# Performance work log

Hardware: AMD Instinct MI355X
Metric: run time of the kernel (lower is better)

## Reference

```python
import jax, jax.numpy as jnp
import numpy as np

EPS = 1e-7  # K.epsilon()
ROUTINGS = 3

def squash(x, axis=-1):
    s2 = jnp.sum(jnp.square(x), axis=axis, keepdims=True)
    scale = s2 / (1.0 + s2) / jnp.sqrt(s2 + EPS)
    return scale * x

def setup_inputs() -> dict:
    key = jax.random.key(0)
    k1, k2 = jax.random.split(key)
    B, N, Di = 64, 1152, 16   # batch, n_input_capsules, dim_input_capsule
    C, Dc = 32, 32            # n_capsules, dim_capsule
    inputs = jax.random.normal(k1, (B, N, Di), dtype=jnp.float32)
    # glorot-style scale for stability
    W = jax.random.normal(k2, (C, N, Dc, Di), dtype=jnp.float32) * (1.0 / np.sqrt(Di))
    return {"inputs": inputs, "W": W}

def reference(inputs, W):
    # inputs: [B, N, Di]; W: [C, N, Dc, Di]
    # inputs_hat[b,c,n,j] = sum_i inputs[b,n,i] * W[c,n,j,i]
    u_hat = jnp.einsum('bni,cnji->bcnj', inputs, W)  # [B, C, N, Dc]
    B, C, N, Dc = u_hat.shape
    b = jnp.zeros((B, C, N), dtype=u_hat.dtype)
    outputs = None
    for i in range(ROUTINGS):
        c = jax.nn.softmax(b, axis=1)                 # softmax over output capsules
        s = jnp.einsum('bcn,bcnj->bcj', c, u_hat)     # weighted sum over input caps
        outputs = squash(s)                           # [B, C, Dc]
        if i < ROUTINGS - 1:
            b = b + jnp.einsum('bcj,bcnj->bcn', outputs, u_hat)
    return outputs
```

## Files before the change

kernel.cpp:

```cpp
#include <hip/hip_runtime.h>
#include <math.h>

using bh8    = __attribute__((ext_vector_type(8))) short;
using f32x16 = __attribute__((ext_vector_type(16))) float;
typedef unsigned int u32;

#define NN   1152
#define CCAP 32
#define DI   16
#define DCAP 32
#define TNR  9
#define NTILES 128
#define CAPS_EPS 1e-7f

#define LDS_W    0
#define LDS_X    65536
#define LDS_DU   74752
#define LDS_CF   78976
#define LDS_TOT  83200

#define WS_WB    0ul
#define WS_XB    37748736ul
#define WS_PART  40108032ul
#define WS_PART2 73662464ul
#define WS_OPK   77856768ul
#define WS_BLOG  77987840ul

__device__ __forceinline__ short f2bf(float f) {
    u32 u = __float_as_uint(f);
    u += 0x7fffu + ((u >> 16) & 1u);
    return (short)(u >> 16);
}

__device__ __forceinline__ void gld_lds16(const void* g, void* s) {
    __builtin_amdgcn_global_load_lds(
        (const __attribute__((address_space(1))) u32*)g,
        (__attribute__((address_space(3))) u32*)s, 16, 0, 0);
}

__global__ __launch_bounds__(256)
void conv_w(const float* __restrict__ W, short* __restrict__ Wb)
{
    const int m = blockIdx.x * 256 + threadIdx.x;
    const int l = m & 63, c = (m >> 6) & 31, n = m >> 11;
    const int j = l & 31, hi = l >> 5;
    const float* src = W + (((size_t)c * NN + n) * DCAP + j) * DI + hi * 8;
    const float4 a = ((const float4*)src)[0];
    const float4 b = ((const float4*)src)[1];
    bh8 r;
    r[0] = f2bf(a.x); r[1] = f2bf(a.y); r[2] = f2bf(a.z); r[3] = f2bf(a.w);
    r[4] = f2bf(b.x); r[5] = f2bf(b.y); r[6] = f2bf(b.z); r[7] = f2bf(b.w);
    *(bh8*)(Wb + (size_t)m * 8) = r;
}

__global__ __launch_bounds__(256)
void conv_x(const float* __restrict__ X, short* __restrict__ xb)
{
    const int m = blockIdx.x * 256 + threadIdx.x;
    const int l = m & 63;
    const int h = m / (NN * 64);
    const int n = (m >> 6) % NN;
    const int b = h * 32 + (l & 31), hi = l >> 5;
    const float* src = X + ((size_t)b * NN + n) * DI + hi * 8;
    const float4 a = ((const float4*)src)[0];
    const float4 c4 = ((const float4*)src)[1];
    bh8 r;
    r[0] = f2bf(a.x);  r[1] = f2bf(a.y);  r[2] = f2bf(a.z);  r[3] = f2bf(a.w);
    r[4] = f2bf(c4.x); r[5] = f2bf(c4.y); r[6] = f2bf(c4.z); r[7] = f2bf(c4.w);
    *(bh8*)(xb + (size_t)m * 8) = r;
}

template<int T>
__global__ __launch_bounds__(512, 2)
void route_k(const short* __restrict__ Wb, const short* __restrict__ xb,
             const u32* __restrict__ opk, float* __restrict__ blog,
             float* __restrict__ part)
{
    extern __shared__ char smem[];
    const int tid = threadIdx.x;
    const int w = tid >> 6, l = tid & 63, bl31 = l & 31;
    const int nt = blockIdx.x, h = blockIdx.y;
    const int n0 = nt * TNR;
    const int bk = h * NTILES + nt;

    char* Wl  = smem + LDS_W;
    char* Xl  = smem + LDS_X;
    float* DU = (float*)(smem + LDS_DU);
    float* CF = (float*)(smem + LDS_CF);

    {
        const char* xs = (const char*)(xb + ((size_t)h * NN + n0) * 512);
        gld_lds16(xs + tid * 16, Xl + tid * 16);
        if (tid < 64) gld_lds16(xs + (512 + tid) * 16, Xl + (512 + tid) * 16);
    }
    {
        const char* wsrc = (const char*)(Wb + (size_t)n0 * 16384);
#pragma unroll
        for (int k = 0; k < 4; ++k)
            gld_lds16(wsrc + (k * 512 + tid) * 16, Wl + (k * 512 + tid) * 16);
    }

    uint4 opr[4][2];
    if (T > 0) {
#pragma unroll
        for (int cc = 0; cc < 4; ++cc) {
            const int c = w * 4 + cc;
            const char* ob = (const char*)opk;
            opr[cc][0] = *(const uint4*)(ob + ((((size_t)h * CCAP + c) * 2 + 0) * 64 + l) * 16);
            opr[cc][1] = *(const uint4*)(ob + ((((size_t)h * CCAP + c) * 2 + 1) * 64 + l) * 16);
        }
    }
    __syncthreads();

    f32x16 sacc[4];
#pragma unroll
    for (int cc = 0; cc < 4; ++cc)
#pragma unroll
        for (int r = 0; r < 16; ++r) sacc[cc][r] = 0.f;

    for (int n = 0; n < TNR; ++n) {
        const int buf = n & 1;
        const int na = n0 + n;

        if (n + 1 < TNR) {
            const char* wsrc = (const char*)(Wb + (size_t)(na + 1) * 16384);
            char* wdst = Wl + (buf ^ 1) * 32768;
#pragma unroll
            for (int k = 0; k < 4; ++k)
                gld_lds16(wsrc + (k * 512 + tid) * 16, wdst + (k * 512 + tid) * 16);
        }

        const bh8 xf = *(const bh8*)(Xl + n * 1024 + l * 16);
        bh8 wf[4];
#pragma unroll
        for (int cc = 0; cc < 4; ++cc) {
            const int c = w * 4 + cc;
            wf[cc] = *(const bh8*)(Wl + buf * 32768 + (c * 64 + l) * 16);
        }

        if (T == 0) {
#pragma unroll
            for (int cc = 0; cc < 4; ++cc)
                sacc[cc] = __builtin_amdgcn_mfma_f32_32x32x16_bf16(wf[cc], xf, sacc[cc], 0, 0, 0);
        } else {
            f32x16 zz;
#pragma unroll
            for (int r = 0; r < 16; ++r) zz[r] = 0.f;
            f32x16 u[4];
#pragma unroll
            for (int cc = 0; cc < 4; ++cc)
                u[cc] = __builtin_amdgcn_mfma_f32_32x32x16_bf16(wf[cc], xf, zz, 0, 0, 0);

            float du[4];
#pragma unroll
            for (int cc = 0; cc < 4; ++cc) {
                const u32 o[8] = {opr[cc][0].x, opr[cc][0].y, opr[cc][0].z, opr[cc][0].w,
                                  opr[cc][1].x, opr[cc][1].y, opr[cc][1].z, opr[cc][1].w};
                float d = 0.f;
#pragma unroll
                for (int p = 0; p < 8; ++p) {
                    const float e0 = __uint_as_float(o[p] << 16);
                    const float e1 = __uint_as_float(o[p] & 0xffff0000u);
                    d = fmaf(e0, u[cc][2 * p + 0], d);
                    d = fmaf(e1, u[cc][2 * p + 1], d);
                }
                d += __shfl_xor(d, 32);
                const int c = w * 4 + cc;
                if (T == 2) d += blog[(((size_t)na * CCAP + c) * 2 + h) * 32 + bl31];
                du[cc] = d;
            }
#pragma unroll
            for (int cc = 0; cc < 4; ++cc) {
                const int c = w * 4 + cc;
                if (l < 32) {
                    DU[c * 33 + l] = du[cc];
                    if (T == 1) blog[(((size_t)na * CCAP + c) * 2 + h) * 32 + l] = du[cc];
                }
            }
            __syncthreads();

            {
                const int b = tid >> 4, g = tid & 15;
                const float v0 = DU[g * 33 + b], v1 = DU[(g + 16) * 33 + b];
                float m = fmaxf(v0, v1);
#pragma unroll
                for (int d2 = 1; d2 < 16; d2 <<= 1) m = fmaxf(m, __shfl_xor(m, d2));
                const float e0 = __expf(v0 - m), e1 = __expf(v1 - m);
                float es = e0 + e1;
#pragma unroll
                for (int d2 = 1; d2 < 16; d2 <<= 1) es += __shfl_xor(es, d2);
                const float inv = 1.0f / es;
                CF[g * 33 + b] = e0 * inv;
                CF[(g + 16) * 33 + b] = e1 * inv;
            }
            __syncthreads();

#pragma unroll
            for (int cc = 0; cc < 4; ++cc) {
                const int c = w * 4 + cc;
                const float cf = CF[c * 33 + bl31];
#pragma unroll
                for (int r = 0; r < 16; ++r)
                    sacc[cc][r] = fmaf(cf, u[cc][r], sacc[cc][r]);
            }
        }
        if (T == 0) __syncthreads();
    }

#pragma unroll
    for (int cc = 0; cc < 4; ++cc) {
        const int c = w * 4 + cc;
        float* dst = part + (((size_t)bk * CCAP + c) * 64 + l) * 16;
#pragma unroll
        for (int k = 0; k < 4; ++k) {
            float4 v;
            v.x = sacc[cc][4 * k + 0]; v.y = sacc[cc][4 * k + 1];
            v.z = sacc[cc][4 * k + 2]; v.w = sacc[cc][4 * k + 3];
            ((float4*)dst)[k] = v;
        }
    }
}

__global__ __launch_bounds__(1024)
void reduce1_k(const float* __restrict__ part, float* __restrict__ part2)
{
    const int t = threadIdx.x;
    const int ch = blockIdx.x, c = blockIdx.y, h = blockIdx.z;
    float a = 0.f;
#pragma unroll
    for (int s = 0; s < 8; ++s) {
        const int nt = ch * 8 + s;
        a += part[((size_t)(h * NTILES + nt) * CCAP + c) * 1024 + t];
    }
    part2[(((size_t)h * CCAP + c) * 16 + ch) * 1024 + t] = a;
}

template<int FIN>
__global__ __launch_bounds__(1024)
void reduce2_k(const float* __restrict__ part2, u32* __restrict__ opk,
               float* __restrict__ outp, float sc0)
{
    const int t = threadIdx.x;
    const int c = blockIdx.x, h = blockIdx.y;
    const int l = t >> 4, r = t & 15;
    float s = 0.f;
#pragma unroll
    for (int ch = 0; ch < 16; ++ch)
        s += part2[(((size_t)h * CCAP + c) * 16 + ch) * 1024 + t];
    s *= sc0;

    float q = s * s;
    q += __shfl_xor(q, 1); q += __shfl_xor(q, 2);
    q += __shfl_xor(q, 4); q += __shfl_xor(q, 8);
    __shared__ float ssq[64], scl[32];
    if (r == 0) ssq[l] = q;
    __syncthreads();
    if (t < 32) {
        const float v = ssq[t] + ssq[t + 32];
        scl[t] = v / ((1.0f + v) * sqrtf(v + CAPS_EPS));
    }
    __syncthreads();
    const float o = s * scl[l & 31];

    if (FIN) {
        const int b = h * 32 + (l & 31);
        const int j = (r & 3) + 8 * (r >> 2) + 4 * (l >> 5);
        outp[((size_t)b * CCAP + c) * DCAP + j] = o;
    } else {
        const float o1 = __shfl_xor(o, 1);
        if (!(r & 1)) {
            const u32 pk = (u32)(unsigned short)f2bf(o) |
                           ((u32)(unsigned short)f2bf(o1) << 16);
            opk[((((size_t)h * CCAP + c) * 2 + (r >> 3)) * 64 + l) * 4 + ((r >> 1) & 3)] = pk;
        }
    }
}

extern "C" void kernel_launch(void* const* d_in, const int* in_sizes, int n_in,
                              void* d_out, int out_size, void* d_ws, size_t ws_size,
                              hipStream_t stream)
{
    const float* inp = (const float*)d_in[0];
    const float* Wt  = (const float*)d_in[1];
    float* out = (float*)d_out;

    char* ws = (char*)d_ws;
    short* Wb    = (short*)(ws + WS_WB);
    short* xb    = (short*)(ws + WS_XB);
    float* part  = (float*)(ws + WS_PART);
    float* part2 = (float*)(ws + WS_PART2);
    u32*   opk   = (u32*)  (ws + WS_OPK);
    float* blog  = (float*)(ws + WS_BLOG);

    hipFuncSetAttribute((const void*)route_k<0>, hipFuncAttributeMaxDynamicSharedMemorySize, LDS_TOT);
    hipFuncSetAttribute((const void*)route_k<1>, hipFuncAttributeMaxDynamicSharedMemorySize, LDS_TOT);
    hipFuncSetAttribute((const void*)route_k<2>, hipFuncAttributeMaxDynamicSharedMemorySize, LDS_TOT);

    conv_w<<<9216, 256, 0, stream>>>(Wt, Wb);
    conv_x<<<576, 256, 0, stream>>>(inp, xb);

    const dim3 gr(NTILES, 2), br(512);
    const dim3 g1(16, 32, 2);
    const dim3 g2(32, 2);

    route_k<0><<<gr, br, LDS_TOT, stream>>>(Wb, xb, opk, blog, part);
    reduce1_k<<<g1, 1024, 0, stream>>>(part, part2);
    reduce2_k<0><<<g2, 1024, 0, stream>>>(part2, opk, out, 1.0f / 32.0f);

    route_k<1><<<gr, br, LDS_TOT, stream>>>(Wb, xb, opk, blog, part);
    reduce1_k<<<g1, 1024, 0, stream>>>(part, part2);
    reduce2_k<0><<<g2, 1024, 0, stream>>>(part2, opk, out, 1.0f);

    route_k<2><<<gr, br, LDS_TOT, stream>>>(Wb, xb, opk, blog, part);
    reduce1_k<<<g1, 1024, 0, stream>>>(part, part2);
    reduce2_k<1><<<g2, 1024, 0, stream>>>(part2, opk, out, 1.0f);
}
```

Measured before the change: 217.3 us.

## Load W fragments directly to registers and double threads per routing block

The routing kernel stops staging W tiles through double-buffered LDS and instead loads each wave's W fragments straight from global memory into registers, prefetching the next input capsule's fragments. Blocks grow from 512 to 1024 threads, with each wave handling two output capsules instead of four. LDS shrinks to the x tile plus the softmax scratch, which lowers register pressure per wave and raises occupancy. In exchange, W loads no longer use async LDS copies, so global latency must be hidden by the register prefetch and the extra waves. The block-wide barriers now span twice as many waves.

```diff
diff --git a/kernel.cpp b/kernel.cpp
--- a/kernel.cpp
+++ b/kernel.cpp
@@ -12,12 +12,6 @@
 #define TNR  9
 #define NTILES 128
 #define CAPS_EPS 1e-7f
-
-#define LDS_W    0
-#define LDS_X    65536
-#define LDS_DU   74752
-#define LDS_CF   78976
-#define LDS_TOT  83200
 
 #define WS_WB    0ul
 #define WS_XB    37748736ul
@@ -71,115 +65,98 @@
 }
 
 template<int T>
-__global__ __launch_bounds__(512, 2)
+__global__ __launch_bounds__(1024, 4)
 void route_k(const short* __restrict__ Wb, const short* __restrict__ xb,
              const u32* __restrict__ opk, float* __restrict__ blog,
              float* __restrict__ part)
 {
-    extern __shared__ char smem[];
+    __shared__ __align__(16) char Xl[TNR * 1024];
+    __shared__ float DU[CCAP * 33];
+    __shared__ float CF[CCAP * 33];
+
     const int tid = threadIdx.x;
     const int w = tid >> 6, l = tid & 63, bl31 = l & 31;
     const int nt = blockIdx.x, h = blockIdx.y;
     const int n0 = nt * TNR;
     const int bk = h * NTILES + nt;
-
-    char* Wl  = smem + LDS_W;
-    char* Xl  = smem + LDS_X;
-    float* DU = (float*)(smem + LDS_DU);
-    float* CF = (float*)(smem + LDS_CF);
-
-    {
+    const int c0 = w * 2, c1 = c0 + 1;
+
+    if (tid < TNR * 64) {
         const char* xs = (const char*)(xb + ((size_t)h * NN + n0) * 512);
         gld_lds16(xs + tid * 16, Xl + tid * 16);
-        if (tid < 64) gld_lds16(xs + (512 + tid) * 16, Xl + (512 + tid) * 16);
-    }
+    }
+
+    uint4 opr[2][2];
+    if (T > 0) {
+        const char* ob = (const char*)opk;
+        opr[0][0] = *(const uint4*)(ob + ((((size_t)h * CCAP + c0) * 2 + 0) * 64 + l) * 16);
+        opr[0][1] = *(const uint4*)(ob + ((((size_t)h * CCAP + c0) * 2 + 1) * 64 + l) * 16);
+        opr[1][0] = *(const uint4*)(ob + ((((size_t)h * CCAP + c1) * 2 + 0) * 64 + l) * 16);
+        opr[1][1] = *(const uint4*)(ob + ((((size_t)h * CCAP + c1) * 2 + 1) * 64 + l) * 16);
+    }
+
+    bh8 wA0, wA1, wB0, wB1;
     {
-        const char* wsrc = (const char*)(Wb + (size_t)n0 * 16384);
-#pragma unroll
-        for (int k = 0; k < 4; ++k)
-            gld_lds16(wsrc + (k * 512 + tid) * 16, Wl + (k * 512 + tid) * 16);
-    }
-
-    uint4 opr[4][2];
-    if (T > 0) {
-#pragma unroll
-        for (int cc = 0; cc < 4; ++cc) {
-            const int c = w * 4 + cc;
-            const char* ob = (const char*)opk;
-            opr[cc][0] = *(const uint4*)(ob + ((((size_t)h * CCAP + c) * 2 + 0) * 64 + l) * 16);
-            opr[cc][1] = *(const uint4*)(ob + ((((size_t)h * CCAP + c) * 2 + 1) * 64 + l) * 16);
-        }
-    }
+        const short* p = Wb + (size_t)n0 * 16384;
+        wA0 = *(const bh8*)(p + (c0 * 64 + l) * 8);
+        wA1 = *(const bh8*)(p + (c1 * 64 + l) * 8);
+    }
+
+    f32x16 s0, s1;
+#pragma unroll
+    for (int r = 0; r < 16; ++r) { s0[r] = 0.f; s1[r] = 0.f; }
+
     __syncthreads();
 
-    f32x16 sacc[4];
-#pragma unroll
-    for (int cc = 0; cc < 4; ++cc)
-#pragma unroll
-        for (int r = 0; r < 16; ++r) sacc[cc][r] = 0.f;
-
+#pragma unroll
     for (int n = 0; n < TNR; ++n) {
-        const int buf = n & 1;
         const int na = n0 + n;
 
         if (n + 1 < TNR) {
-            const char* wsrc = (const char*)(Wb + (size_t)(na + 1) * 16384);
-            char* wdst = Wl + (buf ^ 1) * 32768;
-#pragma unroll
-            for (int k = 0; k < 4; ++k)
-                gld_lds16(wsrc + (k * 512 + tid) * 16, wdst + (k * 512 + tid) * 16);
+            const short* p = Wb + (size_t)(na + 1) * 16384;
+            wB0 = *(const bh8*)(p + (c0 * 64 + l) * 8);
+            wB1 = *(const bh8*)(p + (c1 * 64 + l) * 8);
         }
 
         const bh8 xf = *(const bh8*)(Xl + n * 1024 + l * 16);
-        bh8 wf[4];
-#pragma unroll
-        for (int cc = 0; cc < 4; ++cc) {
-            const int c = w * 4 + cc;
-            wf[cc] = *(const bh8*)(Wl + buf * 32768 + (c * 64 + l) * 16);
-        }
 
         if (T == 0) {
-#pragma unroll
-            for (int cc = 0; cc < 4; ++cc)
-                sacc[cc] = __builtin_amdgcn_mfma_f32_32x32x16_bf16(wf[cc], xf, sacc[cc], 0, 0, 0);
+            s0 = __builtin_amdgcn_mfma_f32_32x32x16_bf16(wA0, xf, s0, 0, 0, 0);
+            s1 = __builtin_amdgcn_mfma_f32_32x32x16_bf16(wA1, xf, s1, 0, 0, 0);
         } else {
             f32x16 zz;
 #pragma unroll
             for (int r = 0; r < 16; ++r) zz[r] = 0.f;
-            f32x16 u[4];
-#pragma unroll
-            for (int cc = 0; cc < 4; ++cc)
-                u[cc] = __builtin_amdgcn_mfma_f32_32x32x16_bf16(wf[cc], xf, zz, 0, 0, 0);
-
-            float du[4];
-#pragma unroll
-            for (int cc = 0; cc < 4; ++cc) {
-                const u32 o[8] = {opr[cc][0].x, opr[cc][0].y, opr[cc][0].z, opr[cc][0].w,
-                                  opr[cc][1].x, opr[cc][1].y, opr[cc][1].z, opr[cc][1].w};
-                float d = 0.f;
-#pragma unroll
-                for (int p = 0; p < 8; ++p) {
-                    const float e0 = __uint_as_float(o[p] << 16);
-                    const float e1 = __uint_as_float(o[p] & 0xffff0000u);
-                    d = fmaf(e0, u[cc][2 * p + 0], d);
-                    d = fmaf(e1, u[cc][2 * p + 1], d);
+            f32x16 u0 = __builtin_amdgcn_mfma_f32_32x32x16_bf16(wA0, xf, zz, 0, 0, 0);
+            f32x16 u1 = __builtin_amdgcn_mfma_f32_32x32x16_bf16(wA1, xf, zz, 0, 0, 0);
+
+            float d0 = 0.f, d1 = 0.f;
+#pragma unroll
+            for (int p = 0; p < 8; ++p) {
+                const u32 o0 = (p < 4) ? (&opr[0][0].x)[p] : (&opr[0][1].x)[p - 4];
+                const u32 o1 = (p < 4) ? (&opr[1][0].x)[p] : (&opr[1][1].x)[p - 4];
+                d0 = fmaf(__uint_as_float(o0 << 16),        u0[2 * p + 0], d0);
+                d0 = fmaf(__uint_as_float(o0 & 0xffff0000u), u0[2 * p + 1], d0);
+                d1 = fmaf(__uint_as_float(o1 << 16),        u1[2 * p + 0], d1);
+                d1 = fmaf(__uint_as_float(o1 & 0xffff0000u), u1[2 * p + 1], d1);
+            }
+            d0 += __shfl_xor(d0, 32);
+            d1 += __shfl_xor(d1, 32);
+            if (T == 2) {
+                d0 += blog[(((size_t)na * CCAP + c0) * 2 + h) * 32 + bl31];
+                d1 += blog[(((size_t)na * CCAP + c1) * 2 + h) * 32 + bl31];
+            }
+            if (l < 32) {
+                DU[c0 * 33 + l] = d0;
+                DU[c1 * 33 + l] = d1;
+                if (T == 1) {
+                    blog[(((size_t)na * CCAP + c0) * 2 + h) * 32 + l] = d0;
+                    blog[(((size_t)na * CCAP + c1) * 2 + h) * 32 + l] = d1;
                 }
-                d += __shfl_xor(d, 32);
-                const int c = w * 4 + cc;
-                if (T == 2) d += blog[(((size_t)na * CCAP + c) * 2 + h) * 32 + bl31];
-                du[cc] = d;
-            }
-#pragma unroll
-            for (int cc = 0; cc < 4; ++cc) {
-                const int c = w * 4 + cc;
-                if (l < 32) {
-                    DU[c * 33 + l] = du[cc];
-                    if (T == 1) blog[(((size_t)na * CCAP + c) * 2 + h) * 32 + l] = du[cc];
-                }
             }
             __syncthreads();
 
-            {
+            if (tid < 512) {
                 const int b = tid >> 4, g = tid & 15;
                 const float v0 = DU[g * 33 + b], v1 = DU[(g + 16) * 33 + b];
                 float m = fmaxf(v0, v1);
@@ -195,28 +172,27 @@
             }
             __syncthreads();
 
-#pragma unroll
-            for (int cc = 0; cc < 4; ++cc) {
-                const int c = w * 4 + cc;
-                const float cf = CF[c * 33 + bl31];
-#pragma unroll
-                for (int r = 0; r < 16; ++r)
-                    sacc[cc][r] = fmaf(cf, u[cc][r], sacc[cc][r]);
-            }
-        }
-        if (T == 0) __syncthreads();
-    }
-
-#pragma unroll
-    for (int cc = 0; cc < 4; ++cc) {
-        const int c = w * 4 + cc;
-        float* dst = part + (((size_t)bk * CCAP + c) * 64 + l) * 16;
+            const float cf0 = CF[c0 * 33 + bl31];
+            const float cf1 = CF[c1 * 33 + bl31];
+#pragma unroll
+            for (int r = 0; r < 16; ++r) {
+                s0[r] = fmaf(cf0, u0[r], s0[r]);
+                s1[r] = fmaf(cf1, u1[r], s1[r]);
+            }
+        }
+        wA0 = wB0; wA1 = wB1;
+    }
+
+    {
+        float* dst0 = part + (((size_t)bk * CCAP + c0) * 64 + l) * 16;
+        float* dst1 = part + (((size_t)bk * CCAP + c1) * 64 + l) * 16;
 #pragma unroll
         for (int k = 0; k < 4; ++k) {
-            float4 v;
-            v.x = sacc[cc][4 * k + 0]; v.y = sacc[cc][4 * k + 1];
-            v.z = sacc[cc][4 * k + 2]; v.w = sacc[cc][4 * k + 3];
-            ((float4*)dst)[k] = v;
+            float4 v0, v1;
+            v0.x = s0[4 * k]; v0.y = s0[4 * k + 1]; v0.z = s0[4 * k + 2]; v0.w = s0[4 * k + 3];
+            v1.x = s1[4 * k]; v1.y = s1[4 * k + 1]; v1.z = s1[4 * k + 2]; v1.w = s1[4 * k + 3];
+            ((float4*)dst0)[k] = v0;
+            ((float4*)dst1)[k] = v1;
         }
     }
 }
@@ -292,26 +268,22 @@
     u32*   opk   = (u32*)  (ws + WS_OPK);
     float* blog  = (float*)(ws + WS_BLOG);
 
-    hipFuncSetAttribute((const void*)route_k<0>, hipFuncAttributeMaxDynamicSharedMemorySize, LDS_TOT);
-    hipFuncSetAttribute((const void*)route_k<1>, hipFuncAttributeMaxDynamicSharedMemorySize, LDS_TOT);
-    hipFuncSetAttribute((const void*)route_k<2>, hipFuncAttributeMaxDynamicSharedMemorySize, LDS_TOT);
-
     conv_w<<<9216, 256, 0, stream>>>(Wt, Wb);
     conv_x<<<576, 256, 0, stream>>>(inp, xb);
 
-    const dim3 gr(NTILES, 2), br(512);
+    const dim3 gr(NTILES, 2), br(1024);
     const dim3 g1(16, 32, 2);
     const dim3 g2(32, 2);
 
-    route_k<0><<<gr, br, LDS_TOT, stream>>>(Wb, xb, opk, blog, part);
+    route_k<0><<<gr, br, 0, stream>>>(Wb, xb, opk, blog, part);
     reduce1_k<<<g1, 1024, 0, stream>>>(part, part2);
     reduce2_k<0><<<g2, 1024, 0, stream>>>(part2, opk, out, 1.0f / 32.0f);
 
-    route_k<1><<<gr, br, LDS_TOT, stream>>>(Wb, xb, opk, blog, part);
+    route_k<1><<<gr, br, 0, stream>>>(Wb, xb, opk, blog, part);
     reduce1_k<<<g1, 1024, 0, stream>>>(part, part2);
     reduce2_k<0><<<g2, 1024, 0, stream>>>(part2, opk, out, 1.0f);
 
-    route_k<2><<<gr, br, LDS_TOT, stream>>>(Wb, xb, opk, blog, part);
+    route_k<2><<<gr, br, 0, stream>>>(Wb, xb, opk, blog, part);
     reduce1_k<<<g1, 1024, 0, stream>>>(part, part2);
     reduce2_k<1><<<g2, 1024, 0, stream>>>(part2, opk, out, 1.0f);
 }
```

After: 513.9 us. +136.5%, slower.

## Stream W fragments directly into registers and recompute MFMA instead of holding u

Applied to the files above, without the earlier changes.

Drops the LDS double buffer for the bf16 weights and prefetches each wave's W fragments straight from global memory into registers, one step ahead. In the routing passes it recomputes the u_hat MFMA after the softmax rather than keeping four 16-float accumulators live, which lowers register pressure. It also merges the W and X bf16 conversion kernels into one launch and removes the trailing barrier from the T==0 loop. In exchange it does extra MFMA work and relies on register prefetch to hide global latency, while the much smaller static LDS use may change occupancy.

```diff
diff --git a/kernel.cpp b/kernel.cpp
--- a/kernel.cpp
+++ b/kernel.cpp
@@ -13,12 +13,6 @@
 #define NTILES 128
 #define CAPS_EPS 1e-7f
 
-#define LDS_W    0
-#define LDS_X    65536
-#define LDS_DU   74752
-#define LDS_CF   78976
-#define LDS_TOT  83200
-
 #define WS_WB    0ul
 #define WS_XB    37748736ul
 #define WS_PART  40108032ul
@@ -39,139 +33,126 @@
 }
 
 __global__ __launch_bounds__(256)
-void conv_w(const float* __restrict__ W, short* __restrict__ Wb)
-{
-    const int m = blockIdx.x * 256 + threadIdx.x;
-    const int l = m & 63, c = (m >> 6) & 31, n = m >> 11;
-    const int j = l & 31, hi = l >> 5;
-    const float* src = W + (((size_t)c * NN + n) * DCAP + j) * DI + hi * 8;
-    const float4 a = ((const float4*)src)[0];
-    const float4 b = ((const float4*)src)[1];
-    bh8 r;
-    r[0] = f2bf(a.x); r[1] = f2bf(a.y); r[2] = f2bf(a.z); r[3] = f2bf(a.w);
-    r[4] = f2bf(b.x); r[5] = f2bf(b.y); r[6] = f2bf(b.z); r[7] = f2bf(b.w);
-    *(bh8*)(Wb + (size_t)m * 8) = r;
-}
-
-__global__ __launch_bounds__(256)
-void conv_x(const float* __restrict__ X, short* __restrict__ xb)
-{
-    const int m = blockIdx.x * 256 + threadIdx.x;
-    const int l = m & 63;
-    const int h = m / (NN * 64);
-    const int n = (m >> 6) % NN;
-    const int b = h * 32 + (l & 31), hi = l >> 5;
-    const float* src = X + ((size_t)b * NN + n) * DI + hi * 8;
-    const float4 a = ((const float4*)src)[0];
-    const float4 c4 = ((const float4*)src)[1];
-    bh8 r;
-    r[0] = f2bf(a.x);  r[1] = f2bf(a.y);  r[2] = f2bf(a.z);  r[3] = f2bf(a.w);
-    r[4] = f2bf(c4.x); r[5] = f2bf(c4.y); r[6] = f2bf(c4.z); r[7] = f2bf(c4.w);
-    *(bh8*)(xb + (size_t)m * 8) = r;
+void conv_wx(const float* __restrict__ W, const float* __restrict__ X,
+             short* __restrict__ Wb, short* __restrict__ xb)
+{
+    const int bid = blockIdx.x;
+    if (bid < 9216) {
+        const int m = bid * 256 + threadIdx.x;
+        const int l = m & 63, c = (m >> 6) & 31, n = m >> 11;
+        const int j = l & 31, hi = l >> 5;
+        const float* src = W + (((size_t)c * NN + n) * DCAP + j) * DI + hi * 8;
+        const float4 a = ((const float4*)src)[0];
+        const float4 b = ((const float4*)src)[1];
+        bh8 r;
+        r[0] = f2bf(a.x); r[1] = f2bf(a.y); r[2] = f2bf(a.z); r[3] = f2bf(a.w);
+        r[4] = f2bf(b.x); r[5] = f2bf(b.y); r[6] = f2bf(b.z); r[7] = f2bf(b.w);
+        *(bh8*)(Wb + (size_t)m * 8) = r;
+    } else {
+        const int m = (bid - 9216) * 256 + threadIdx.x;
+        const int l = m & 63;
+        const int h = m / (NN * 64);
+        const int n = (m >> 6) % NN;
+        const int b = h * 32 + (l & 31), hi = l >> 5;
+        const float* src = X + ((size_t)b * NN + n) * DI + hi * 8;
+        const float4 a = ((const float4*)src)[0];
+        const float4 c4 = ((const float4*)src)[1];
+        bh8 r;
+        r[0] = f2bf(a.x);  r[1] = f2bf(a.y);  r[2] = f2bf(a.z);  r[3] = f2bf(a.w);
+        r[4] = f2bf(c4.x); r[5] = f2bf(c4.y); r[6] = f2bf(c4.z); r[7] = f2bf(c4.w);
+        *(bh8*)(xb + (size_t)m * 8) = r;
+    }
 }
 
 template<int T>
-__global__ __launch_bounds__(512, 2)
+__global__ __launch_bounds__(512)
 void route_k(const short* __restrict__ Wb, const short* __restrict__ xb,
              const u32* __restrict__ opk, float* __restrict__ blog,
              float* __restrict__ part)
 {
-    extern __shared__ char smem[];
+    __shared__ __align__(16) char Xl[TNR * 1024];
+    __shared__ float DU[CCAP * 33];
+    __shared__ float CF[CCAP * 33];
+
     const int tid = threadIdx.x;
     const int w = tid >> 6, l = tid & 63, bl31 = l & 31;
     const int nt = blockIdx.x, h = blockIdx.y;
     const int n0 = nt * TNR;
     const int bk = h * NTILES + nt;
 
-    char* Wl  = smem + LDS_W;
-    char* Xl  = smem + LDS_X;
-    float* DU = (float*)(smem + LDS_DU);
-    float* CF = (float*)(smem + LDS_CF);
-
     {
         const char* xs = (const char*)(xb + ((size_t)h * NN + n0) * 512);
         gld_lds16(xs + tid * 16, Xl + tid * 16);
         if (tid < 64) gld_lds16(xs + (512 + tid) * 16, Xl + (512 + tid) * 16);
     }
-    {
-        const char* wsrc = (const char*)(Wb + (size_t)n0 * 16384);
-#pragma unroll
-        for (int k = 0; k < 4; ++k)
-            gld_lds16(wsrc + (k * 512 + tid) * 16, Wl + (k * 512 + tid) * 16);
-    }
 
     uint4 opr[4][2];
     if (T > 0) {
+        const char* ob = (const char*)opk;
 #pragma unroll
         for (int cc = 0; cc < 4; ++cc) {
             const int c = w * 4 + cc;
-            const char* ob = (const char*)opk;
             opr[cc][0] = *(const uint4*)(ob + ((((size_t)h * CCAP + c) * 2 + 0) * 64 + l) * 16);
             opr[cc][1] = *(const uint4*)(ob + ((((size_t)h * CCAP + c) * 2 + 1) * 64 + l) * 16);
         }
     }
+
+    bh8 wA[4], wB[4];
+    {
+        const short* p = Wb + (size_t)n0 * 16384;
+#pragma unroll
+        for (int cc = 0; cc < 4; ++cc)
+            wA[cc] = *(const bh8*)(p + ((w * 4 + cc) * 64 + l) * 8);
+    }
+
+    f32x16 sacc[4];
+#pragma unroll
+    for (int cc = 0; cc < 4; ++cc)
+#pragma unroll
+        for (int r = 0; r < 16; ++r) sacc[cc][r] = 0.f;
+
     __syncthreads();
 
-    f32x16 sacc[4];
-#pragma unroll
-    for (int cc = 0; cc < 4; ++cc)
-#pragma unroll
-        for (int r = 0; r < 16; ++r) sacc[cc][r] = 0.f;
-
+#pragma unroll
     for (int n = 0; n < TNR; ++n) {
-        const int buf = n & 1;
         const int na = n0 + n;
 
         if (n + 1 < TNR) {
-            const char* wsrc = (const char*)(Wb + (size_t)(na + 1) * 16384);
-            char* wdst = Wl + (buf ^ 1) * 32768;
-#pragma unroll
-            for (int k = 0; k < 4; ++k)
-                gld_lds16(wsrc + (k * 512 + tid) * 16, wdst + (k * 512 + tid) * 16);
+            const short* p = Wb + (size_t)(na + 1) * 16384;
+#pragma unroll
+            for (int cc = 0; cc < 4; ++cc)
+                wB[cc] = *(const bh8*)(p + ((w * 4 + cc) * 64 + l) * 8);
         }
 
         const bh8 xf = *(const bh8*)(Xl + n * 1024 + l * 16);
-        bh8 wf[4];
-#pragma unroll
-        for (int cc = 0; cc < 4; ++cc) {
-            const int c = w * 4 + cc;
-            wf[cc] = *(const bh8*)(Wl + buf * 32768 + (c * 64 + l) * 16);
-        }
 
         if (T == 0) {
 #pragma unroll
             for (int cc = 0; cc < 4; ++cc)
-                sacc[cc] = __builtin_amdgcn_mfma_f32_32x32x16_bf16(wf[cc], xf, sacc[cc], 0, 0, 0);
+                sacc[cc] = __builtin_amdgcn_mfma_f32_32x32x16_bf16(wA[cc], xf, sacc[cc], 0, 0, 0);
         } else {
             f32x16 zz;
 #pragma unroll
             for (int r = 0; r < 16; ++r) zz[r] = 0.f;
-            f32x16 u[4];
-#pragma unroll
-            for (int cc = 0; cc < 4; ++cc)
-                u[cc] = __builtin_amdgcn_mfma_f32_32x32x16_bf16(wf[cc], xf, zz, 0, 0, 0);
 
             float du[4];
 #pragma unroll
             for (int cc = 0; cc < 4; ++cc) {
-                const u32 o[8] = {opr[cc][0].x, opr[cc][0].y, opr[cc][0].z, opr[cc][0].w,
-                                  opr[cc][1].x, opr[cc][1].y, opr[cc][1].z, opr[cc][1].w};
+                const f32x16 ut = __builtin_amdgcn_mfma_f32_32x32x16_bf16(wA[cc], xf, zz, 0, 0, 0);
                 float d = 0.f;
 #pragma unroll
                 for (int p = 0; p < 8; ++p) {
-                    const float e0 = __uint_as_float(o[p] << 16);
-                    const float e1 = __uint_as_float(o[p] & 0xffff0000u);
-                    d = fmaf(e0, u[cc][2 * p + 0], d);
-                    d = fmaf(e1, u[cc][2 * p + 1], d);
+                    const u32 o = (p < 4) ? (&opr[cc][0].x)[p] : (&opr[cc][1].x)[p - 4];
+                    d = fmaf(__uint_as_float(o << 16),         ut[2 * p + 0], d);
+                    d = fmaf(__uint_as_float(o & 0xffff0000u), ut[2 * p + 1], d);
                 }
-                d += __shfl_xor(d, 32);
+                du[cc] = d;
+            }
+#pragma unroll
+            for (int cc = 0; cc < 4; ++cc) {
+                du[cc] += __shfl_xor(du[cc], 32);
                 const int c = w * 4 + cc;
-                if (T == 2) d += blog[(((size_t)na * CCAP + c) * 2 + h) * 32 + bl31];
-                du[cc] = d;
-            }
-#pragma unroll
-            for (int cc = 0; cc < 4; ++cc) {
-                const int c = w * 4 + cc;
+                if (T == 2) du[cc] += blog[(((size_t)na * CCAP + c) * 2 + h) * 32 + bl31];
                 if (l < 32) {
                     DU[c * 33 + l] = du[cc];
                     if (T == 1) blog[(((size_t)na * CCAP + c) * 2 + h) * 32 + l] = du[cc];
@@ -194,23 +175,23 @@
                 CF[(g + 16) * 33 + b] = e1 * inv;
             }
             __syncthreads();
+            __builtin_amdgcn_sched_barrier(0);
 
 #pragma unroll
             for (int cc = 0; cc < 4; ++cc) {
-                const int c = w * 4 + cc;
-                const float cf = CF[c * 33 + bl31];
-#pragma unroll
-                for (int r = 0; r < 16; ++r)
-                    sacc[cc][r] = fmaf(cf, u[cc][r], sacc[cc][r]);
-            }
-        }
-        if (T == 0) __syncthreads();
+                const float cf = CF[(w * 4 + cc) * 33 + bl31];
+                const f32x16 ut = __builtin_amdgcn_mfma_f32_32x32x16_bf16(wA[cc], xf, zz, 0, 0, 0);
+#pragma unroll
+                for (int r = 0; r < 16; ++r) sacc[cc][r] = fmaf(cf, ut[r], sacc[cc][r]);
+            }
+        }
+#pragma unroll
+        for (int cc = 0; cc < 4; ++cc) wA[cc] = wB[cc];
     }
 
 #pragma unroll
     for (int cc = 0; cc < 4; ++cc) {
-        const int c = w * 4 + cc;
-        float* dst = part + (((size_t)bk * CCAP + c) * 64 + l) * 16;
+        float* dst = part + (((size_t)bk * CCAP + w * 4 + cc) * 64 + l) * 16;
 #pragma unroll
         for (int k = 0; k < 4; ++k) {
             float4 v;
@@ -292,26 +273,21 @@
     u32*   opk   = (u32*)  (ws + WS_OPK);
     float* blog  = (float*)(ws + WS_BLOG);
 
-    hipFuncSetAttribute((const void*)route_k<0>, hipFuncAttributeMaxDynamicSharedMemorySize, LDS_TOT);
-    hipFuncSetAttribute((const void*)route_k<1>, hipFuncAttributeMaxDynamicSharedMemorySize, LDS_TOT);
-    hipFuncSetAttribute((const void*)route_k<2>, hipFuncAttributeMaxDynamicSharedMemorySize, LDS_TOT);
-
-    conv_w<<<9216, 256, 0, stream>>>(Wt, Wb);
-    conv_x<<<576, 256, 0, stream>>>(inp, xb);
+    conv_wx<<<9792, 256, 0, stream>>>(Wt, inp, Wb, xb);
 
     const dim3 gr(NTILES, 2), br(512);
     const dim3 g1(16, 32, 2);
     const dim3 g2(32, 2);
 
-    route_k<0><<<gr, br, LDS_TOT, stream>>>(Wb, xb, opk, blog, part);
+    route_k<0><<<gr, br, 0, stream>>>(Wb, xb, opk, blog, part);
     reduce1_k<<<g1, 1024, 0, stream>>>(part, part2);
     reduce2_k<0><<<g2, 1024, 0, stream>>>(part2, opk, out, 1.0f / 32.0f);
 
-    route_k<1><<<gr, br, LDS_TOT, stream>>>(Wb, xb, opk, blog, part);
+    route_k<1><<<gr, br, 0, stream>>>(Wb, xb, opk, blog, part);
     reduce1_k<<<g1, 1024, 0, stream>>>(part, part2);
     reduce2_k<0><<<g2, 1024, 0, stream>>>(part2, opk, out, 1.0f);
 
-    route_k<2><<<gr, br, LDS_TOT, stream>>>(Wb, xb, opk, blog, part);
+    route_k<2><<<gr, br, 0, stream>>>(Wb, xb, opk, blog, part);
     reduce1_k<<<g1, 1024, 0, stream>>>(part, part2);
     reduce2_k<1><<<g2, 1024, 0, stream>>>(part2, opk, out, 1.0f);
 }
```

After: 590.9 us. 172% more time.
